# Optimization experiments

Hardware: AMD Instinct MI355X
Metric: run time of the kernel (lower is better)

Reference implementation:

```python
import jax, jax.numpy as jnp
import numpy as np

N_NODES = 100000
N_EDGES = 1600000
F_IN = 8
PERIODS = 18
UNITS = 256     # A3TGCN out_channels (unit_num)
HIDDEN = 256    # MLP hidden_units


def setup_inputs() -> dict:
    key = jax.random.key(0)
    ks = jax.random.split(key, 24)
    g = lambda k, shape, s: (jax.random.normal(k, shape, dtype=jnp.float32) * s)
    inp = {
        "x": g(ks[0], (N_NODES, F_IN, PERIODS), 1.0),
        "edge_index": jax.random.randint(ks[1], (2, N_EDGES), 0, N_NODES, dtype=jnp.int64),
        "edge_weight": jax.random.uniform(ks[2], (N_EDGES,), dtype=jnp.float32),
        # TGCN gate params: GCNConv weight/bias + Linear(2*UNITS, UNITS)
        "Wz": g(ks[3], (F_IN, UNITS), 0.1), "bz": jnp.zeros((UNITS,), jnp.float32),
        "Wlz": g(ks[4], (2 * UNITS, UNITS), 0.05), "blz": jnp.zeros((UNITS,), jnp.float32),
        "Wr": g(ks[5], (F_IN, UNITS), 0.1), "br": jnp.zeros((UNITS,), jnp.float32),
        "Wlr": g(ks[6], (2 * UNITS, UNITS), 0.05), "blr": jnp.zeros((UNITS,), jnp.float32),
        "Wh": g(ks[7], (F_IN, UNITS), 0.1), "bh": jnp.zeros((UNITS,), jnp.float32),
        "Wlh": g(ks[8], (2 * UNITS, UNITS), 0.05), "blh": jnp.zeros((UNITS,), jnp.float32),
        # temporal attention logits
        "att": jax.random.uniform(ks[9], (PERIODS,), dtype=jnp.float32),
        # MLP head
        "W1": g(ks[10], (UNITS, HIDDEN), 0.05), "b1": jnp.zeros((HIDDEN,), jnp.float32),
        "W2": g(ks[11], (HIDDEN, HIDDEN), 0.05), "b2": jnp.zeros((HIDDEN,), jnp.float32),
        "W3": g(ks[12], (HIDDEN, HIDDEN), 0.05), "b3": jnp.zeros((HIDDEN,), jnp.float32),
        "Wo": g(ks[13], (HIDDEN, PERIODS), 0.05), "bo": jnp.zeros((PERIODS,), jnp.float32),
    }
    return inp


def _gcn_norm(edge_index, edge_weight, n_nodes):
    # PyG gcn_norm with add_self_loops=True, improved=False
    src, dst = edge_index[0], edge_index[1]
    loop = jnp.arange(n_nodes, dtype=src.dtype)
    src_a = jnp.concatenate([src, loop])
    dst_a = jnp.concatenate([dst, loop])
    w_a = jnp.concatenate([edge_weight, jnp.ones((n_nodes,), edge_weight.dtype)])
    deg = jax.ops.segment_sum(w_a, dst_a, num_segments=n_nodes)
    dinv = jnp.where(deg > 0, jax.lax.rsqrt(jnp.where(deg > 0, deg, 1.0)), 0.0)
    norm = dinv[src_a] * w_a * dinv[dst_a]
    return src_a, dst_a, norm


def reference(x, edge_index, edge_weight, Wz, bz, Wlz, blz, Wr, br, Wlr, blr,
              Wh, bh, Wlh, blh, att, W1, b1, W2, b2, W3, b3, Wo, bo):
    n_nodes = x.shape[0]
    src, dst, norm = _gcn_norm(edge_index, edge_weight, n_nodes)

    def gconv(X, W, b):
        m = (X @ W)[src] * norm[:, None]                       # [E+N, UNITS]
        return jax.ops.segment_sum(m, dst, num_segments=n_nodes) + b

    probs = jax.nn.softmax(att)

    def step(carry, inp):
        H, acc = carry
        Xt, p = inp                                            # Xt: [N, F_IN]
        Z = jax.nn.sigmoid(jnp.concatenate([gconv(Xt, Wz, bz), H], 1) @ Wlz + blz)
        R = jax.nn.sigmoid(jnp.concatenate([gconv(Xt, Wr, br), H], 1) @ Wlr + blr)
        Ht = jnp.tanh(jnp.concatenate([gconv(Xt, Wh, bh), H * R], 1) @ Wlh + blh)
        H = Z * H + (1.0 - Z) * Ht
        return (H, acc + p * H), None

    xs = jnp.transpose(x, (2, 0, 1))                           # [T, N, F_IN]
    init = (jnp.zeros((n_nodes, UNITS), x.dtype), jnp.zeros((n_nodes, UNITS), x.dtype))
    (_, h), _ = jax.lax.scan(step, init, (xs, probs))

    h = jax.nn.relu(h)
    h = jax.nn.relu(h @ W1 + b1)
    h = jax.nn.relu(h @ W2 + b2)
    h = jax.nn.relu(h @ W3 + b3)
    return h @ Wo + bo                                         # [N, PERIODS]
```

## Files before the change

kernel.cpp:

```cpp
#include <hip/hip_runtime.h>

typedef _Float16 h8 __attribute__((ext_vector_type(8)));
typedef _Float16 h2 __attribute__((ext_vector_type(2)));
typedef float f4 __attribute__((ext_vector_type(4)));

#define N_NODES 100000
#define NPAD    100096
#define N_EDGES 1600000
#define T_P  18
#define U    256
#define KP   288
#define LDW  296
#define NB_SCAN 391

#define LOG2E  1.44269504f
#define LOG2E2 2.88539008f

__global__ void k_init_deg(float* deg){
    int i = blockIdx.x*256 + threadIdx.x;
    if (i < N_NODES) deg[i] = 1.0f;
}
__global__ void k_deg(const int* __restrict__ ei, const float* __restrict__ w, float* deg){
    int e = blockIdx.x*256 + threadIdx.x;
    if (e < N_EDGES) atomicAdd(&deg[ei[N_EDGES + e]], w[e]);
}
__global__ void k_dinv(const float* deg, float* dinv){
    int i = blockIdx.x*256 + threadIdx.x;
    if (i < N_NODES) dinv[i] = rsqrtf(deg[i]);
}
__global__ void k_count(const int* __restrict__ ei, int* cnt){
    int e = blockIdx.x*256 + threadIdx.x;
    if (e < N_EDGES) atomicAdd(&cnt[ei[N_EDGES + e]], 1);
}
__global__ void k_partial(const int* __restrict__ cnt, int* part){
    __shared__ int red[256];
    int b = blockIdx.x, i = b*256 + threadIdx.x;
    red[threadIdx.x] = (i < N_NODES) ? cnt[i] : 0;
    __syncthreads();
    for (int d = 128; d > 0; d >>= 1){
        if (threadIdx.x < d) red[threadIdx.x] += red[threadIdx.x + d];
        __syncthreads();
    }
    if (threadIdx.x == 0) part[b] = red[0];
}
__global__ void k_scan_part(const int* __restrict__ part, int* pbase){
    __shared__ int s[512];
    int tid = threadIdx.x;
    int v = (tid < NB_SCAN) ? part[tid] : 0;
    s[tid] = v; __syncthreads();
    for (int d = 1; d < 512; d <<= 1){
        int t2 = (tid >= d) ? s[tid - d] : 0;
        __syncthreads();
        s[tid] += t2;
        __syncthreads();
    }
    if (tid < NB_SCAN) pbase[tid] = s[tid] - v;
}
__global__ void k_emit(const int* __restrict__ cnt, const int* __restrict__ pbase,
                       int* rowp, int* ccur){
    __shared__ int s[256];
    int b = blockIdx.x, tid = threadIdx.x, i = b*256 + tid;
    int v = (i < N_NODES) ? cnt[i] : 0;
    s[tid] = v; __syncthreads();
    for (int d = 1; d < 256; d <<= 1){
        int t2 = (tid >= d) ? s[tid - d] : 0;
        __syncthreads();
        s[tid] += t2;
        __syncthreads();
    }
    int excl = s[tid] - v + pbase[b];
    if (i < N_NODES){
        rowp[i] = excl; ccur[i] = excl;
        if (i == N_NODES - 1) rowp[N_NODES] = excl + v;
    }
}
__global__ void k_scatter(const int* __restrict__ ei, const float* __restrict__ w,
                          const float* __restrict__ dinv, int* ccur,
                          int* __restrict__ csrc, float* __restrict__ cnrm){
    int e = blockIdx.x*256 + threadIdx.x;
    if (e >= N_EDGES) return;
    int s = ei[e], d = ei[N_EDGES + e];
    int pos = atomicAdd(&ccur[d], 1);
    csrc[pos] = s;
    cnrm[pos] = dinv[s] * w[e] * dinv[d];
}
__global__ void k_gather_nf(const float* __restrict__ x, const float* __restrict__ dinv,
                            const int* __restrict__ rowp, const int* __restrict__ csrc,
                            const float* __restrict__ cnrm, _Float16* __restrict__ AXh){
    int idx = blockIdx.x*256 + threadIdx.x;
    if (idx >= N_NODES*8) return;
    int n = idx >> 3, f = idx & 7;
    float dv = dinv[n];
    float w0 = dv * dv;
    const float* xb = x + (size_t)n*144 + f*18;
    float s[T_P];
    #pragma unroll
    for (int t = 0; t < T_P; t++) s[t] = w0 * xb[t];
    int p1 = rowp[n+1];
    for (int p = rowp[n]; p < p1; p++){
        float w = cnrm[p];
        const float* xs = x + (size_t)csrc[p]*144 + f*18;
        #pragma unroll
        for (int t = 0; t < T_P; t++) s[t] += w * xs[t];
    }
    #pragma unroll
    for (int t = 0; t < T_P; t++)
        AXh[((size_t)t*NPAD + n)*8 + f] = (_Float16)s[t];
}

__global__ void k_probs(const float* att, float* probs){
    if (threadIdx.x == 0 && blockIdx.x == 0){
        float mx = -1e30f;
        for (int t = 0; t < T_P; t++) mx = fmaxf(mx, att[t]);
        float e[T_P], s = 0.f;
        for (int t = 0; t < T_P; t++){ e[t] = __expf(att[t] - mx); s += e[t]; }
        for (int t = 0; t < T_P; t++) probs[t] = e[t] / s;
    }
}
__global__ void k_wprime(const float* Wz, const float* bz, const float* Wlz, const float* blz,
                         const float* Wr, const float* br, const float* Wlr, const float* blr,
                         const float* Wh, const float* bh, const float* Wlh, const float* blh,
                         float* wprime, float* biasg){
    int idx = blockIdx.x*256 + threadIdx.x;
    if (idx >= 3*9*256) return;
    int g = idx / (9*256); int rem = idx - g*9*256;
    int row = rem / 256;   int u = rem - row*256;
    const float* W  = g==0 ? Wz  : (g==1 ? Wr  : Wh);
    const float* Wl = g==0 ? Wlz : (g==1 ? Wlr : Wlh);
    const float* bb = g==0 ? bz  : (g==1 ? br  : bh);
    const float* bl = g==0 ? blz : (g==1 ? blr : blh);
    float s = 0.f;
    if (row < 8){
        for (int c = 0; c < U; c++) s += W[row*U + c] * Wl[c*U + u];
        wprime[(g*8 + row)*U + u] = s;
    } else {
        for (int c = 0; c < U; c++) s += bb[c] * Wl[c*U + u];
        biasg[g*U + u] = s + bl[u];
    }
}
__global__ void k_fill_gates(const float* __restrict__ wprime, const float* __restrict__ Wlz,
                             const float* __restrict__ Wlr, const float* __restrict__ Wlh,
                             _Float16* __restrict__ B1t, _Float16* __restrict__ B2t){
    int idx = blockIdx.x*256 + threadIdx.x;
    if (idx >= 768*KP) return;
    int n = idx / KP, k = idx - n*KP;
    int g = (n < 256) ? 0 : ((n < 512) ? 1 : 2);
    int u = n & 255;
    const float* Wl = g==0 ? Wlz : (g==1 ? Wlr : Wlh);
    float v;
    if (k < 8)        v = wprime[(g*8 + k)*U + u];
    else if (k < 264) v = Wl[(256 + (k - 8))*U + u];
    else              v = 0.f;
    if (n < 512) B1t[(size_t)n*KP + k] = (_Float16)v;
    else         B2t[(size_t)(n - 512)*KP + k] = (_Float16)v;
}
__global__ void k_fill_mlp(const float* __restrict__ W1, const float* __restrict__ W2,
                           const float* __restrict__ W3, const float* __restrict__ Wo,
                           _Float16* W1t, _Float16* W2t, _Float16* W3t, _Float16* WoT){
    int idx = blockIdx.x*256 + threadIdx.x;
    if (idx >= 3*U*KP + 64*KP) return;
    if (idx < 3*U*KP){
        int l = idx / (U*KP); int rem = idx - l*U*KP;
        int n = rem / KP, k = rem - n*KP;
        const float* W = l==0 ? W1 : (l==1 ? W2 : W3);
        _Float16*   Wt = l==0 ? W1t : (l==1 ? W2t : W3t);
        Wt[(size_t)n*KP + k] = (k >= 8 && k < 264) ? (_Float16)W[(size_t)(k-8)*U + n] : (_Float16)0.f;
    } else {
        int rem = idx - 3*U*KP;
        int n = rem / KP, k = rem - n*KP;
        WoT[(size_t)n*KP + k] = (n < T_P && k >= 8 && k < 264) ? (_Float16)Wo[(size_t)(k-8)*T_P + n] : (_Float16)0.f;
    }
}

__device__ __forceinline__ void gemm_pass(const _Float16* sbuf, const _Float16* __restrict__ Bg,
                                          int brow, int lr, int lq, f4* g){
    for (int kt = 0; kt < 9; kt++){
        h8 af[4], bf[2];
        #pragma unroll
        for (int i = 0; i < 4; i++)
            af[i] = *(const h8*)(sbuf + (i*16 + lr)*LDW + kt*32 + lq*8);
        #pragma unroll
        for (int j = 0; j < 2; j++)
            bf[j] = *(const h8*)(Bg + (size_t)(brow + j*16 + lr)*KP + kt*32 + lq*8);
        #pragma unroll
        for (int i = 0; i < 4; i++)
            #pragma unroll
            for (int j = 0; j < 2; j++)
                g[i*2 + j] = __builtin_amdgcn_mfma_f32_16x16x32_f16(af[i], bf[j], g[i*2 + j], 0, 0, 0);
    }
}
__device__ __forceinline__ void gemm_pass2(const _Float16* sbuf, const _Float16* __restrict__ Bg,
                                           int browZ, int browR, int lr, int lq, f4* gz, f4* gr){
    for (int kt = 0; kt < 9; kt++){
        h8 af[4], bz_[2], br_[2];
        #pragma unroll
        for (int i = 0; i < 4; i++)
            af[i] = *(const h8*)(sbuf + (i*16 + lr)*LDW + kt*32 + lq*8);
        #pragma unroll
        for (int j = 0; j < 2; j++){
            bz_[j] = *(const h8*)(Bg + (size_t)(browZ + j*16 + lr)*KP + kt*32 + lq*8);
            br_[j] = *(const h8*)(Bg + (size_t)(browR + j*16 + lr)*KP + kt*32 + lq*8);
        }
        #pragma unroll
        for (int i = 0; i < 4; i++)
            #pragma unroll
            for (int j = 0; j < 2; j++){
                gz[i*2 + j] = __builtin_amdgcn_mfma_f32_16x16x32_f16(af[i], bz_[j], gz[i*2 + j], 0, 0, 0);
                gr[i*2 + j] = __builtin_amdgcn_mfma_f32_16x16x32_f16(af[i], br_[j], gr[i*2 + j], 0, 0, 0);
            }
    }
}

__global__ __attribute__((amdgpu_waves_per_eu(2, 4))) __launch_bounds__(512)
void k_fused(const _Float16* __restrict__ AXh,
             const _Float16* __restrict__ B1t, const _Float16* __restrict__ B2t,
             const float* __restrict__ biasg,
             const _Float16* __restrict__ W1t, const _Float16* __restrict__ W2t,
             const _Float16* __restrict__ W3t, const _Float16* __restrict__ WoT,
             const float* __restrict__ b1, const float* __restrict__ b2,
             const float* __restrict__ b3, const float* __restrict__ bo,
             const float* __restrict__ probs, float* __restrict__ dout){
    __shared__ __align__(16) _Float16 sA[64*LDW];
    __shared__ __align__(16) _Float16 sB[64*LDW];
    const int tid  = threadIdx.x;
    const int wave = tid >> 6, lane = tid & 63;
    const int lr = lane & 15, lq = lane >> 4;
    const int wc = wave * 32;
    const int n0 = blockIdx.x * 64;

    {
        uint* w0 = (uint*)sA; uint* w1 = (uint*)sB;
        for (int i = tid; i < 64*LDW/2; i += 512){ w0[i] = 0u; w1[i] = 0u; }
    }
    __syncthreads();
    if (tid < 64)
        *(uint4*)(&sA[tid*LDW]) = *(const uint4*)(AXh + ((size_t)0*NPAD + n0 + tid)*8);

    float bz_r[2], br_r[2], bh_r[2];
    #pragma unroll
    for (int j = 0; j < 2; j++){
        int col = wc + j*16 + lr;
        bz_r[j] = -LOG2E  * biasg[col];
        br_r[j] = -LOG2E  * biasg[256 + col];
        bh_r[j] =  LOG2E2 * biasg[512 + col];
    }

    h2 acc[16], hr[16];
    h2 z2 = {(_Float16)0.f, (_Float16)0.f};
    #pragma unroll
    for (int k = 0; k < 16; k++){ acc[k] = z2; hr[k] = z2; }

    const f4 fz = {0.f, 0.f, 0.f, 0.f};
    __syncthreads();

    for (int t = 0; t < T_P; t++){
        const float pt = probs[t];
        const int last = (t == T_P - 1);
        uint4 ld;
        if (tid < 64){
            if (!last) ld = *(const uint4*)(AXh + ((size_t)(t+1)*NPAD + n0 + tid)*8);
        } else if (tid < 128){
            ld = *(const uint4*)(AXh + ((size_t)t*NPAD + n0 + (tid-64))*8);
        }
        f4 gz[8], gr[8];
        #pragma unroll
        for (int k = 0; k < 8; k++){ gz[k] = fz; gr[k] = fz; }
        gemm_pass2(sA, B1t, wc, 256 + wc, lr, lq, gz, gr);
        #pragma unroll
        for (int i = 0; i < 4; i++)
            #pragma unroll
            for (int j = 0; j < 2; j++)
                #pragma unroll
                for (int r = 0; r < 4; r++){
                    int v = (i*2 + j)*4 + r;
                    int row = i*16 + lq*4 + r;
                    int col = wc + j*16 + lr;
                    float rr = __builtin_amdgcn_rcpf(
                        1.f + __builtin_amdgcn_exp2f(fmaf(gr[i*2 + j][r], -LOG2E, br_r[j])));
                    sB[row*LDW + 8 + col] = (_Float16)((float)hr[v>>1][v&1] * rr);
                }
        if (tid >= 64 && tid < 128)
            *(uint4*)(&sB[(tid-64)*LDW]) = ld;
        __syncthreads();
        f4 g[8];
        #pragma unroll
        for (int k = 0; k < 8; k++) g[k] = fz;
        gemm_pass(sB, B2t, wc, lr, lq, g);
        #pragma unroll
        for (int i = 0; i < 4; i++)
            #pragma unroll
            for (int j = 0; j < 2; j++)
                #pragma unroll
                for (int r = 0; r < 4; r++){
                    int v = (i*2 + j)*4 + r;
                    int row = i*16 + lq*4 + r;
                    int col = wc + j*16 + lr;
                    float e2 = __builtin_amdgcn_exp2f(fmaf(g[i*2 + j][r], LOG2E2, bh_r[j]));
                    float ht = fmaf(-2.f, __builtin_amdgcn_rcpf(e2 + 1.f), 1.f);
                    float z  = __builtin_amdgcn_rcpf(
                        1.f + __builtin_amdgcn_exp2f(fmaf(gz[i*2 + j][r], -LOG2E, bz_r[j])));
                    float h  = (float)hr[v>>1][v&1];
                    float hn = fmaf(z, h - ht, ht);
                    float a  = fmaf(pt, hn, (float)acc[v>>1][v&1]);
                    acc[v>>1][v&1] = (_Float16)a;
                    hr[v>>1][v&1]  = (_Float16)hn;
                    sA[row*LDW + 8 + col] = (_Float16)(last ? fmaxf(a, 0.f) : hn);
                }
        if (!last && tid < 64)
            *(uint4*)(&sA[tid*LDW]) = ld;
        __syncthreads();
    }

    #pragma unroll
    for (int l = 0; l < 3; l++){
        const _Float16* Wt = (l == 0) ? W1t : (l == 1) ? W2t : W3t;
        const float*    bl = (l == 0) ? b1  : (l == 1) ? b2  : b3;
        float blv[2];
        #pragma unroll
        for (int j = 0; j < 2; j++) blv[j] = bl[wc + j*16 + lr];
        f4 g[8];
        #pragma unroll
        for (int k = 0; k < 8; k++) g[k] = fz;
        gemm_pass(sA, Wt, wc, lr, lq, g);
        __syncthreads();
        #pragma unroll
        for (int i = 0; i < 4; i++)
            #pragma unroll
            for (int j = 0; j < 2; j++)
                #pragma unroll
                for (int r = 0; r < 4; r++){
                    int row = i*16 + lq*4 + r;
                    int col = wc + j*16 + lr;
                    sA[row*LDW + 8 + col] = (_Float16)fmaxf(g[i*2 + j][r] + blv[j], 0.f);
                }
        __syncthreads();
    }
    if (wave == 0){
        f4 g[8];
        #pragma unroll
        for (int k = 0; k < 8; k++) g[k] = fz;
        gemm_pass(sA, WoT, 0, lr, lq, g);
        #pragma unroll
        for (int i = 0; i < 4; i++)
            #pragma unroll
            for (int j = 0; j < 2; j++)
                #pragma unroll
                for (int r = 0; r < 4; r++){
                    int row = i*16 + lq*4 + r;
                    int col = j*16 + lr;
                    int gm = n0 + row;
                    if (col < T_P && gm < N_NODES)
                        dout[(size_t)gm*T_P + col] = g[i*2 + j][r] + bo[col];
                }
    }
}

extern "C" void kernel_launch(void* const* d_in, const int* in_sizes, int n_in,
                              void* d_out, int out_size, void* d_ws, size_t ws_size,
                              hipStream_t stream){
    const float* x   = (const float*)d_in[0];
    const int*   ei  = (const int*)  d_in[1];
    const float* ew  = (const float*)d_in[2];
    const float* Wz  = (const float*)d_in[3];  const float* bz  = (const float*)d_in[4];
    const float* Wlz = (const float*)d_in[5];  const float* blz = (const float*)d_in[6];
    const float* Wr  = (const float*)d_in[7];  const float* br  = (const float*)d_in[8];
    const float* Wlr = (const float*)d_in[9];  const float* blr = (const float*)d_in[10];
    const float* Wh  = (const float*)d_in[11]; const float* bh  = (const float*)d_in[12];
    const float* Wlh = (const float*)d_in[13]; const float* blh = (const float*)d_in[14];
    const float* att = (const float*)d_in[15];
    const float* W1  = (const float*)d_in[16]; const float* b1  = (const float*)d_in[17];
    const float* W2  = (const float*)d_in[18]; const float* b2  = (const float*)d_in[19];
    const float* W3  = (const float*)d_in[20]; const float* b3  = (const float*)d_in[21];
    const float* Wo  = (const float*)d_in[22]; const float* bo  = (const float*)d_in[23];
    float* dout = (float*)d_out;

    char* ws = (char*)d_ws; size_t off = 0;
    auto alloc = [&](size_t bytes)->char*{ char* p = ws + off; off += (bytes + 255) & ~(size_t)255; return p; };
    _Float16* AXh   = (_Float16*)alloc((size_t)T_P*NPAD*8*2);
    float*    deg   = (float*)alloc((size_t)N_NODES*4);
    float*    dinv  = (float*)alloc((size_t)N_NODES*4);
    int*      cnt   = (int*)  alloc((size_t)N_NODES*4);
    int*      rowp  = (int*)  alloc(((size_t)N_NODES + 1)*4);
    int*      ccur  = (int*)  alloc((size_t)N_NODES*4);
    int*      csrc  = (int*)  alloc((size_t)N_EDGES*4);
    float*    cnrm  = (float*)alloc((size_t)N_EDGES*4);
    int*      part  = (int*)  alloc((size_t)NB_SCAN*4);
    int*      pbase = (int*)  alloc((size_t)NB_SCAN*4);
    float*    wprime= (float*)alloc((size_t)3*8*U*4);
    float*    biasg = (float*)alloc((size_t)3*U*4);
    _Float16* B1t   = (_Float16*)alloc((size_t)512*KP*2);
    _Float16* B2t   = (_Float16*)alloc((size_t)256*KP*2);
    _Float16* W1t   = (_Float16*)alloc((size_t)U*KP*2);
    _Float16* W2t   = (_Float16*)alloc((size_t)U*KP*2);
    _Float16* W3t   = (_Float16*)alloc((size_t)U*KP*2);
    _Float16* WoT   = (_Float16*)alloc((size_t)64*KP*2);
    float*    probs = (float*)alloc((size_t)T_P*4);

    hipMemsetAsync(AXh, 0, (size_t)T_P*NPAD*8*2, stream);
    hipMemsetAsync(cnt, 0, (size_t)N_NODES*4, stream);

    k_probs<<<1, 64, 0, stream>>>(att, probs);
    k_wprime<<<(3*9*256 + 255)/256, 256, 0, stream>>>(Wz,bz,Wlz,blz, Wr,br,Wlr,blr, Wh,bh,Wlh,blh, wprime, biasg);
    k_fill_gates<<<(768*KP + 255)/256, 256, 0, stream>>>(wprime, Wlz, Wlr, Wlh, B1t, B2t);
    k_fill_mlp<<<(3*U*KP + 64*KP + 255)/256, 256, 0, stream>>>(W1, W2, W3, Wo, W1t, W2t, W3t, WoT);

    k_init_deg<<<(N_NODES + 255)/256, 256, 0, stream>>>(deg);
    k_deg<<<(N_EDGES + 255)/256, 256, 0, stream>>>(ei, ew, deg);
    k_dinv<<<(N_NODES + 255)/256, 256, 0, stream>>>(deg, dinv);
    k_count<<<(N_EDGES + 255)/256, 256, 0, stream>>>(ei, cnt);
    k_partial<<<NB_SCAN, 256, 0, stream>>>(cnt, part);
    k_scan_part<<<1, 512, 0, stream>>>(part, pbase);
    k_emit<<<NB_SCAN, 256, 0, stream>>>(cnt, pbase, rowp, ccur);
    k_scatter<<<(N_EDGES + 255)/256, 256, 0, stream>>>(ei, ew, dinv, ccur, csrc, cnrm);
    k_gather_nf<<<(N_NODES*8 + 255)/256, 256, 0, stream>>>(x, dinv, rowp, csrc, cnrm, AXh);

    k_fused<<<NPAD/64, 512, 0, stream>>>(AXh, B1t, B2t, biasg, W1t, W2t, W3t, WoT,
                                         b1, b2, b3, bo, probs, dout);
}
```

Measured before the change: 2.420 ms.

## Split fused kernel tile across 16 waves with 2x2 MFMA subtiles

Doubles the block to 1024 threads and splits the 64-row tile across two row halves, so each wave computes a 32x32 output subtile instead of 64x32. This halves per-wave accumulators and register pressure and aims at more latency hiding within a block. The cost is that each B-matrix (weight) fragment is now loaded from global memory by twice as many waves. An unused htr array is declared and the waves_per_eu hint is dropped.

Result: slower. 4.077 ms (+68.5%).

```diff
diff --git a/kernel.cpp b/kernel.cpp
--- a/kernel.cpp
+++ b/kernel.cpp
@@ -172,46 +172,40 @@
     }
 }
 
-__device__ __forceinline__ void gemm_pass(const _Float16* sbuf, const _Float16* __restrict__ Bg,
-                                          int brow, int lr, int lq, f4* g){
+__device__ __forceinline__ void gemm_22(const _Float16* sbuf, const _Float16* __restrict__ Bg,
+                                        int rbase, int brow, int lr, int lq, f4* g){
     for (int kt = 0; kt < 9; kt++){
-        h8 af[4], bf[2];
-        #pragma unroll
-        for (int i = 0; i < 4; i++)
-            af[i] = *(const h8*)(sbuf + (i*16 + lr)*LDW + kt*32 + lq*8);
-        #pragma unroll
-        for (int j = 0; j < 2; j++)
-            bf[j] = *(const h8*)(Bg + (size_t)(brow + j*16 + lr)*KP + kt*32 + lq*8);
-        #pragma unroll
-        for (int i = 0; i < 4; i++)
-            #pragma unroll
-            for (int j = 0; j < 2; j++)
-                g[i*2 + j] = __builtin_amdgcn_mfma_f32_16x16x32_f16(af[i], bf[j], g[i*2 + j], 0, 0, 0);
-    }
-}
-__device__ __forceinline__ void gemm_pass2(const _Float16* sbuf, const _Float16* __restrict__ Bg,
-                                           int browZ, int browR, int lr, int lq, f4* gz, f4* gr){
+        h8 a0 = *(const h8*)(sbuf + (rbase + lr)*LDW + kt*32 + lq*8);
+        h8 a1 = *(const h8*)(sbuf + (rbase + 16 + lr)*LDW + kt*32 + lq*8);
+        h8 b0 = *(const h8*)(Bg + (size_t)(brow + lr)*KP + kt*32 + lq*8);
+        h8 b1 = *(const h8*)(Bg + (size_t)(brow + 16 + lr)*KP + kt*32 + lq*8);
+        g[0] = __builtin_amdgcn_mfma_f32_16x16x32_f16(a0, b0, g[0], 0, 0, 0);
+        g[1] = __builtin_amdgcn_mfma_f32_16x16x32_f16(a0, b1, g[1], 0, 0, 0);
+        g[2] = __builtin_amdgcn_mfma_f32_16x16x32_f16(a1, b0, g[2], 0, 0, 0);
+        g[3] = __builtin_amdgcn_mfma_f32_16x16x32_f16(a1, b1, g[3], 0, 0, 0);
+    }
+}
+__device__ __forceinline__ void gemm_zr(const _Float16* sbuf, const _Float16* __restrict__ Bg,
+                                        int rbase, int wcc, int lr, int lq, f4* gz, f4* gr){
     for (int kt = 0; kt < 9; kt++){
-        h8 af[4], bz_[2], br_[2];
-        #pragma unroll
-        for (int i = 0; i < 4; i++)
-            af[i] = *(const h8*)(sbuf + (i*16 + lr)*LDW + kt*32 + lq*8);
-        #pragma unroll
-        for (int j = 0; j < 2; j++){
-            bz_[j] = *(const h8*)(Bg + (size_t)(browZ + j*16 + lr)*KP + kt*32 + lq*8);
-            br_[j] = *(const h8*)(Bg + (size_t)(browR + j*16 + lr)*KP + kt*32 + lq*8);
-        }
-        #pragma unroll
-        for (int i = 0; i < 4; i++)
-            #pragma unroll
-            for (int j = 0; j < 2; j++){
-                gz[i*2 + j] = __builtin_amdgcn_mfma_f32_16x16x32_f16(af[i], bz_[j], gz[i*2 + j], 0, 0, 0);
-                gr[i*2 + j] = __builtin_amdgcn_mfma_f32_16x16x32_f16(af[i], br_[j], gr[i*2 + j], 0, 0, 0);
-            }
-    }
-}
-
-__global__ __attribute__((amdgpu_waves_per_eu(2, 4))) __launch_bounds__(512)
+        h8 a0 = *(const h8*)(sbuf + (rbase + lr)*LDW + kt*32 + lq*8);
+        h8 a1 = *(const h8*)(sbuf + (rbase + 16 + lr)*LDW + kt*32 + lq*8);
+        h8 bz0 = *(const h8*)(Bg + (size_t)(wcc + lr)*KP + kt*32 + lq*8);
+        h8 bz1 = *(const h8*)(Bg + (size_t)(wcc + 16 + lr)*KP + kt*32 + lq*8);
+        h8 br0 = *(const h8*)(Bg + (size_t)(256 + wcc + lr)*KP + kt*32 + lq*8);
+        h8 br1 = *(const h8*)(Bg + (size_t)(256 + wcc + 16 + lr)*KP + kt*32 + lq*8);
+        gz[0] = __builtin_amdgcn_mfma_f32_16x16x32_f16(a0, bz0, gz[0], 0, 0, 0);
+        gz[1] = __builtin_amdgcn_mfma_f32_16x16x32_f16(a0, bz1, gz[1], 0, 0, 0);
+        gz[2] = __builtin_amdgcn_mfma_f32_16x16x32_f16(a1, bz0, gz[2], 0, 0, 0);
+        gz[3] = __builtin_amdgcn_mfma_f32_16x16x32_f16(a1, bz1, gz[3], 0, 0, 0);
+        gr[0] = __builtin_amdgcn_mfma_f32_16x16x32_f16(a0, br0, gr[0], 0, 0, 0);
+        gr[1] = __builtin_amdgcn_mfma_f32_16x16x32_f16(a0, br1, gr[1], 0, 0, 0);
+        gr[2] = __builtin_amdgcn_mfma_f32_16x16x32_f16(a1, br0, gr[2], 0, 0, 0);
+        gr[3] = __builtin_amdgcn_mfma_f32_16x16x32_f16(a1, br1, gr[3], 0, 0, 0);
+    }
+}
+
+__global__ __launch_bounds__(1024)
 void k_fused(const _Float16* __restrict__ AXh,
              const _Float16* __restrict__ B1t, const _Float16* __restrict__ B2t,
              const float* __restrict__ biasg,
@@ -225,12 +219,14 @@
     const int tid  = threadIdx.x;
     const int wave = tid >> 6, lane = tid & 63;
     const int lr = lane & 15, lq = lane >> 4;
-    const int wc = wave * 32;
+    const int ri  = wave >> 3;
+    const int rbase = ri * 32;
+    const int wcc = (wave & 7) * 32;
     const int n0 = blockIdx.x * 64;
 
     {
         uint* w0 = (uint*)sA; uint* w1 = (uint*)sB;
-        for (int i = tid; i < 64*LDW/2; i += 512){ w0[i] = 0u; w1[i] = 0u; }
+        for (int i = tid; i < 64*LDW/2; i += 1024){ w0[i] = 0u; w1[i] = 0u; }
     }
     __syncthreads();
     if (tid < 64)
@@ -239,16 +235,16 @@
     float bz_r[2], br_r[2], bh_r[2];
     #pragma unroll
     for (int j = 0; j < 2; j++){
-        int col = wc + j*16 + lr;
+        int col = wcc + j*16 + lr;
         bz_r[j] = -LOG2E  * biasg[col];
         br_r[j] = -LOG2E  * biasg[256 + col];
         bh_r[j] =  LOG2E2 * biasg[512 + col];
     }
 
-    h2 acc[16], hr[16];
+    h2 acc[8], hr[8], htr[8];
     h2 z2 = {(_Float16)0.f, (_Float16)0.f};
     #pragma unroll
-    for (int k = 0; k < 16; k++){ acc[k] = z2; hr[k] = z2; }
+    for (int k = 0; k < 8; k++){ acc[k] = z2; hr[k] = z2; }
 
     const f4 fz = {0.f, 0.f, 0.f, 0.f};
     __syncthreads();
@@ -262,39 +258,39 @@
         } else if (tid < 128){
             ld = *(const uint4*)(AXh + ((size_t)t*NPAD + n0 + (tid-64))*8);
         }
-        f4 gz[8], gr[8];
-        #pragma unroll
-        for (int k = 0; k < 8; k++){ gz[k] = fz; gr[k] = fz; }
-        gemm_pass2(sA, B1t, wc, 256 + wc, lr, lq, gz, gr);
-        #pragma unroll
-        for (int i = 0; i < 4; i++)
+        f4 gz[4], gr[4];
+        #pragma unroll
+        for (int k = 0; k < 4; k++){ gz[k] = fz; gr[k] = fz; }
+        gemm_zr(sA, B1t, rbase, wcc, lr, lq, gz, gr);
+        #pragma unroll
+        for (int i = 0; i < 2; i++)
             #pragma unroll
             for (int j = 0; j < 2; j++)
                 #pragma unroll
                 for (int r = 0; r < 4; r++){
                     int v = (i*2 + j)*4 + r;
-                    int row = i*16 + lq*4 + r;
-                    int col = wc + j*16 + lr;
-                    float rr = __builtin_amdgcn_rcpf(
+                    int row = rbase + i*16 + lq*4 + r;
+                    int col = wcc + j*16 + lr;
+                    float rf = __builtin_amdgcn_rcpf(
                         1.f + __builtin_amdgcn_exp2f(fmaf(gr[i*2 + j][r], -LOG2E, br_r[j])));
-                    sB[row*LDW + 8 + col] = (_Float16)((float)hr[v>>1][v&1] * rr);
+                    sB[row*LDW + 8 + col] = (_Float16)((float)hr[v>>1][v&1] * rf);
                 }
         if (tid >= 64 && tid < 128)
             *(uint4*)(&sB[(tid-64)*LDW]) = ld;
         __syncthreads();
-        f4 g[8];
-        #pragma unroll
-        for (int k = 0; k < 8; k++) g[k] = fz;
-        gemm_pass(sB, B2t, wc, lr, lq, g);
-        #pragma unroll
-        for (int i = 0; i < 4; i++)
+        f4 g[4];
+        #pragma unroll
+        for (int k = 0; k < 4; k++) g[k] = fz;
+        gemm_22(sB, B2t, rbase, wcc, lr, lq, g);
+        #pragma unroll
+        for (int i = 0; i < 2; i++)
             #pragma unroll
             for (int j = 0; j < 2; j++)
                 #pragma unroll
                 for (int r = 0; r < 4; r++){
                     int v = (i*2 + j)*4 + r;
-                    int row = i*16 + lq*4 + r;
-                    int col = wc + j*16 + lr;
+                    int row = rbase + i*16 + lq*4 + r;
+                    int col = wcc + j*16 + lr;
                     float e2 = __builtin_amdgcn_exp2f(fmaf(g[i*2 + j][r], LOG2E2, bh_r[j]));
                     float ht = fmaf(-2.f, __builtin_amdgcn_rcpf(e2 + 1.f), 1.f);
                     float z  = __builtin_amdgcn_rcpf(
@@ -317,36 +313,36 @@
         const float*    bl = (l == 0) ? b1  : (l == 1) ? b2  : b3;
         float blv[2];
         #pragma unroll
-        for (int j = 0; j < 2; j++) blv[j] = bl[wc + j*16 + lr];
-        f4 g[8];
-        #pragma unroll
-        for (int k = 0; k < 8; k++) g[k] = fz;
-        gemm_pass(sA, Wt, wc, lr, lq, g);
-        __syncthreads();
-        #pragma unroll
-        for (int i = 0; i < 4; i++)
+        for (int j = 0; j < 2; j++) blv[j] = bl[wcc + j*16 + lr];
+        f4 g[4];
+        #pragma unroll
+        for (int k = 0; k < 4; k++) g[k] = fz;
+        gemm_22(sA, Wt, rbase, wcc, lr, lq, g);
+        __syncthreads();
+        #pragma unroll
+        for (int i = 0; i < 2; i++)
             #pragma unroll
             for (int j = 0; j < 2; j++)
                 #pragma unroll
                 for (int r = 0; r < 4; r++){
-                    int row = i*16 + lq*4 + r;
-                    int col = wc + j*16 + lr;
+                    int row = rbase + i*16 + lq*4 + r;
+                    int col = wcc + j*16 + lr;
                     sA[row*LDW + 8 + col] = (_Float16)fmaxf(g[i*2 + j][r] + blv[j], 0.f);
                 }
         __syncthreads();
     }
-    if (wave == 0){
-        f4 g[8];
-        #pragma unroll
-        for (int k = 0; k < 8; k++) g[k] = fz;
-        gemm_pass(sA, WoT, 0, lr, lq, g);
-        #pragma unroll
-        for (int i = 0; i < 4; i++)
+    if ((wave & 7) == 0){
+        f4 g[4];
+        #pragma unroll
+        for (int k = 0; k < 4; k++) g[k] = fz;
+        gemm_22(sA, WoT, rbase, 0, lr, lq, g);
+        #pragma unroll
+        for (int i = 0; i < 2; i++)
             #pragma unroll
             for (int j = 0; j < 2; j++)
                 #pragma unroll
                 for (int r = 0; r < 4; r++){
-                    int row = i*16 + lq*4 + r;
+                    int row = rbase + i*16 + lq*4 + r;
                     int col = j*16 + lr;
                     int gm = n0 + row;
                     if (col < T_P && gm < N_NODES)
@@ -414,6 +410,6 @@
     k_scatter<<<(N_EDGES + 255)/256, 256, 0, stream>>>(ei, ew, dinv, ccur, csrc, cnrm);
     k_gather_nf<<<(N_NODES*8 + 255)/256, 256, 0, stream>>>(x, dinv, rowp, csrc, cnrm, AXh);
 
-    k_fused<<<NPAD/64, 512, 0, stream>>>(AXh, B1t, B2t, biasg, W1t, W2t, W3t, WoT,
-                                         b1, b2, b3, bo, probs, dout);
-}
+    k_fused<<<NPAD/64, 1024, 0, stream>>>(AXh, B1t, B2t, biasg, W1t, W2t, W3t, WoT,
+                                          b1, b2, b3, bo, probs, dout);
+}
```
